# Kernel tuning notes

Measured on AMD Instinct MI355X. Metric: run time of the kernel, lower is better.

## Reference

```python
import jax, jax.numpy as jnp
import numpy as np

N = 50000          # number of input/output nodes (M == N since out_features=None)
E = 1_600_000      # total neighbor entries (avg degree 32)
C_IN = 64
HID = 128
C_OUT = 64


def setup_inputs() -> dict:
    key = jax.random.key(0)
    k1, k2, k3, k4, k5 = jax.random.split(key, 5)
    in_features = jax.random.normal(k1, (N, C_IN), dtype=jnp.float32)
    # MLP params: Linear(2C->HID), GELU, Linear(HID->C_OUT)
    W1 = jax.random.normal(k2, (2 * C_IN, HID), dtype=jnp.float32) * (1.0 / np.sqrt(2 * C_IN))
    b1 = jnp.zeros((HID,), dtype=jnp.float32)
    W2 = jax.random.normal(k3, (HID, C_OUT), dtype=jnp.float32) * (1.0 / np.sqrt(HID))
    b2 = jnp.zeros((C_OUT,), dtype=jnp.float32)
    neighbors_index = jax.random.randint(k4, (E,), 0, N, dtype=jnp.int64)
    # row_splits: sorted, starts at 0, ends at E (CSR-style ragged offsets)
    inner = jnp.sort(jax.random.randint(k5, (N - 1,), 0, E, dtype=jnp.int64))
    neighbors_row_splits = jnp.concatenate(
        [jnp.zeros((1,), jnp.int64), inner, jnp.full((1,), E, jnp.int64)])
    return {
        "in_features": in_features,
        "W1": W1, "b1": b1, "W2": W2, "b2": b2,
        "neighbors_index": neighbors_index,
        "neighbors_row_splits": neighbors_row_splits,
    }


def reference(in_features, W1, b1, W2, b2, neighbors_index, neighbors_row_splits):
    rs = neighbors_row_splits
    counts = rs[1:] - rs[:-1]                                  # [M] num_reps per row
    # segment id of each edge: row i owns edges [rs[i], rs[i+1])
    seg_ids = jnp.searchsorted(rs[1:], jnp.arange(E), side="right")  # [E]

    rep_features = in_features[neighbors_index]                # gather neighbors [E, C]
    self_features = in_features[seg_ids]                       # repeat_interleave  [E, C]
    agg = jnp.concatenate([rep_features, self_features], axis=1)  # [E, 2C]

    h = jax.nn.gelu(agg @ W1 + b1, approximate=False)          # torch GELU = exact erf
    msg = h @ W2 + b2                                          # [E, C_out]

    summed = jax.ops.segment_sum(msg, seg_ids, num_segments=N)  # [M, C_out]
    denom = jnp.maximum(counts, 1).astype(msg.dtype)[:, None]
    return summed / denom                                       # mean reduction
```

## Files before the change

kernel.cpp:

```cpp
#include <hip/hip_runtime.h>
#include <hip/hip_bf16.h>
#include <math.h>

#define C_IN  64
#define HID   128
#define C_OUT 64

typedef __attribute__((ext_vector_type(8))) short s16x8;
typedef __attribute__((ext_vector_type(4))) float f32x4;
typedef __attribute__((ext_vector_type(2))) float f32x2;

__device__ __forceinline__ f32x2 gelu2(f32x2 x) {
    f32x2 t  = x * x;
    f32x2 p  = t * 0.10294455f + 2.30211462f;
    f32x2 xp = x * p;
    f32x2 E;
    E.x = __builtin_amdgcn_exp2f(xp.x);
    E.y = __builtin_amdgcn_exp2f(xp.y);
    f32x2 Ep = E + 1.0f;
    f32x2 r;
    r.x = __builtin_amdgcn_rcpf(Ep.x);
    r.y = __builtin_amdgcn_rcpf(Ep.y);
    return x - x * r;
}

__device__ __forceinline__ float4 fma4(float s, float4 w, float4 acc) {
    acc.x = fmaf(s, w.x, acc.x); acc.y = fmaf(s, w.y, acc.y);
    acc.z = fmaf(s, w.z, acc.z); acc.w = fmaf(s, w.w, acc.w);
    return acc;
}

__device__ __forceinline__ unsigned pk_bf16(float lo, float hi) {
    union { __hip_bfloat162 v; unsigned u; } cv;
    cv.v = __float22bfloat162_rn(make_float2(lo, hi));
    return cv.u;
}
__device__ __forceinline__ f32x2 unpk2(unsigned p) {
    union { unsigned u; float f; } lo, hi;
    lo.u = p << 16; hi.u = p & 0xffff0000u;
    f32x2 v; v.x = lo.f; v.y = hi.f; return v;
}

#define K1_NODES 64

__global__ __launch_bounds__(512, 2) void precompute_ab(
    const float* __restrict__ X, const float* __restrict__ W1,
    const float* __restrict__ b1, const float* __restrict__ W2,
    const int* __restrict__ rs,
    unsigned* __restrict__ A16, float* __restrict__ B,
    unsigned short* __restrict__ W2T, int* __restrict__ bsplit,
    int N, int E, int G)
{
    __shared__ float W1s[2 * C_IN * HID];
    __shared__ float xs[K1_NODES * C_IN];
    int tid = threadIdx.x;

    for (int i = tid; i < (2 * C_IN * HID) / 4; i += 512)
        ((float4*)W1s)[i] = ((const float4*)W1)[i];

    int base = blockIdx.x * K1_NODES;
    int nLoc = min(K1_NODES, N - base);
    for (int i = tid; i < nLoc * (C_IN / 4); i += 512)
        ((float4*)xs)[i] = ((const float4*)(X + (size_t)base * C_IN))[i];

    if (blockIdx.x == 0) {
        for (int i = tid; i < C_OUT * HID; i += 512) {
            int c = i >> 7, k = i & (HID - 1);
            W2T[i] = (unsigned short)pk_bf16(W2[k * C_OUT + c], 0.f);
        }
    }

    {
        int gi = blockIdx.x * 512 + tid;
        if (gi <= G) {
            int t = (int)(((long long)E * gi) / G);
            int lo = 0, hi = N;
            while (lo < hi) { int mm = (lo + hi) >> 1; if (rs[mm] < t) lo = mm + 1; else hi = mm; }
            bsplit[gi] = lo;
        }
    }

    __syncthreads();

    int quad = (tid & 31) * 4;
    int slot = tid >> 5;
    int s0   = slot * 4;
    if (s0 >= nLoc) return;

    float4 a0 = {}, a1 = {}, a2 = {}, a3 = {};
    float4 b0 = {}, b1r = {}, b2r = {}, b3 = {};

    const float* xr0 = xs + (s0 + 0) * C_IN;
    const float* xr1 = xs + (s0 + 1) * C_IN;
    const float* xr2 = xs + (s0 + 2) * C_IN;
    const float* xr3 = xs + (s0 + 3) * C_IN;

#define K1STEP(c, CMP)                                                      \
    do {                                                                    \
        float4 wa = *(const float4*)&W1s[(c) * HID + quad];                 \
        float4 wb = *(const float4*)&W1s[((c) + C_IN) * HID + quad];        \
        a0 = fma4(xv0.CMP, wa, a0); b0  = fma4(xv0.CMP, wb, b0);            \
        a1 = fma4(xv1.CMP, wa, a1); b1r = fma4(xv1.CMP, wb, b1r);           \
        a2 = fma4(xv2.CMP, wa, a2); b2r = fma4(xv2.CMP, wb, b2r);           \
        a3 = fma4(xv3.CMP, wa, a3); b3  = fma4(xv3.CMP, wb, b3);            \
    } while (0)

#pragma unroll 1
    for (int c4 = 0; c4 < C_IN; c4 += 4) {
        float4 xv0 = *(const float4*)&xr0[c4];
        float4 xv1 = *(const float4*)&xr1[c4];
        float4 xv2 = *(const float4*)&xr2[c4];
        float4 xv3 = *(const float4*)&xr3[c4];
        K1STEP(c4 + 0, x);
        K1STEP(c4 + 1, y);
        K1STEP(c4 + 2, z);
        K1STEP(c4 + 3, w);
    }
#undef K1STEP

    float4 bb = *(const float4*)(b1 + quad);
    b0.x += bb.x;  b0.y += bb.y;  b0.z += bb.z;  b0.w += bb.w;
    b1r.x += bb.x; b1r.y += bb.y; b1r.z += bb.z; b1r.w += bb.w;
    b2r.x += bb.x; b2r.y += bb.y; b2r.z += bb.z; b2r.w += bb.w;
    b3.x += bb.x;  b3.y += bb.y;  b3.z += bb.z;  b3.w += bb.w;

    int adw = (base + s0) * (HID / 2) + (quad >> 1);
    size_t boff = (size_t)(base + s0) * HID + quad;
    if (s0 + 0 < nLoc) {
        uint2 u = { pk_bf16(a0.x, a0.y), pk_bf16(a0.z, a0.w) };
        *(uint2*)(A16 + adw) = u;              *(float4*)(B + boff) = b0;
    }
    if (s0 + 1 < nLoc) {
        uint2 u = { pk_bf16(a1.x, a1.y), pk_bf16(a1.z, a1.w) };
        *(uint2*)(A16 + adw + HID / 2) = u;    *(float4*)(B + boff + HID) = b1r;
    }
    if (s0 + 2 < nLoc) {
        uint2 u = { pk_bf16(a2.x, a2.y), pk_bf16(a2.z, a2.w) };
        *(uint2*)(A16 + adw + HID) = u;        *(float4*)(B + boff + 2 * HID) = b2r;
    }
    if (s0 + 3 < nLoc) {
        uint2 u = { pk_bf16(a3.x, a3.y), pk_bf16(a3.z, a3.w) };
        *(uint2*)(A16 + adw + 3 * (HID / 2)) = u; *(float4*)(B + boff + 3 * HID) = b3;
    }
}

#define EA_WAVES 2

#define EA_ISSUE(P0,P1,P2,P3, g) do { int _s8 = ((g) << 3) + half;            \
    int _i0 = __shfl(idx, _s8);                                               \
    int _i1 = __shfl(idx, _s8 + 2);                                           \
    int _i2 = __shfl(idx, _s8 + 4);                                           \
    int _i3 = __shfl(idx, _s8 + 6);                                           \
    P0 = *(const uint2*)(A8 + ((((unsigned)_i0) << 8) | lb));                 \
    P1 = *(const uint2*)(A8 + ((((unsigned)_i1) << 8) | lb));                 \
    P2 = *(const uint2*)(A8 + ((((unsigned)_i2) << 8) | lb));                 \
    P3 = *(const uint2*)(A8 + ((((unsigned)_i3) << 8) | lb));                 \
} while (0)

#define EA_PROC1(P) do {                                                      \
    acc01 += gelu2(unpk2(P.x) + bb01);                                        \
    acc23 += gelu2(unpk2(P.y) + bb23); } while (0)

#define EA_PROC1M(P, p) do {                                                  \
    float _mk = ((((p) << 1) + half) < m) ? 1.f : 0.f;                        \
    acc01 += gelu2(unpk2(P.x) + bb01) * _mk;                                  \
    acc23 += gelu2(unpk2(P.y) + bb23) * _mk; } while (0)

#define EA_PROCG(P0,P1,P2,P3, g) do {                                         \
    if ((((g) + 1) << 3) <= m) { EA_PROC1(P0); EA_PROC1(P1);                  \
                                 EA_PROC1(P2); EA_PROC1(P3); }                \
    else { int _p = (g) << 2;                                                 \
           EA_PROC1M(P0, _p);                                                 \
           if (((_p + 1) << 1) < m) EA_PROC1M(P1, _p + 1);                    \
           if (((_p + 2) << 1) < m) EA_PROC1M(P2, _p + 2);                    \
           if (((_p + 3) << 1) < m) EA_PROC1M(P3, _p + 3); } } while (0)

__global__ __launch_bounds__(128) void edge_agg(
    const unsigned* __restrict__ A16, const float* __restrict__ B,
    const int* __restrict__ nbr, const int* __restrict__ rs,
    const int* __restrict__ bsplit,
    unsigned* __restrict__ Hout, int N, int E, int G)
{
    int wave = threadIdx.x >> 6, lane = threadIdx.x & 63;
    int half = lane >> 5, l5 = lane & 31;
    const char* A8 = (const char*)A16;
    unsigned lb = (unsigned)(l5 << 3);
    int b = blockIdx.x;

    int r0 = bsplit[b];
    int r1 = (b == G - 1) ? N : bsplit[b + 1];

    int row = r0 + wave;
    if (row >= r1) return;

    int s = rs[row], e = rs[row + 1];
    float4 bb4 = *(const float4*)(B + (size_t)row * HID + l5 * 4);
    int idx = 0;
    if (e > s) { int mn = min(64, e - s); idx = nbr[s + min(lane, mn - 1)]; }

    for (;;) {
        int cnt = e - s;

        int nrow = row + EA_WAVES;
        bool hasn = nrow < r1;
        int sn = s, en = e;
        float4 bbn = bb4;
        if (hasn) {
            sn = rs[nrow]; en = rs[nrow + 1];
            bbn = *(const float4*)(B + (size_t)nrow * HID + l5 * 4);
        }

        f32x2 bb01, bb23;
        bb01.x = bb4.x; bb01.y = bb4.y; bb23.x = bb4.z; bb23.y = bb4.w;
        f32x2 acc01 = {0.f, 0.f}, acc23 = {0.f, 0.f};

        if (cnt > 0) {
            int cs = s;
            for (;;) {
                int m = min(64, e - cs);
                int ng = (m + 7) >> 3;

                uint2 A0, A1, A2, A3, B0, B1, B2, B3, C0, C1, C2, C3;
                EA_ISSUE(A0, A1, A2, A3, 0);
                if (ng > 1) EA_ISSUE(B0, B1, B2, B3, 1);

                int ncs = cs + 64;
                int idx_next = idx;
                if (ncs < e) {
                    int mn = min(64, e - ncs);
                    idx_next = nbr[ncs + min(lane, mn - 1)];
                } else if (hasn && en > sn) {
                    int mn = min(64, en - sn);
                    idx_next = nbr[sn + min(lane, mn - 1)];
                }

                int g = 0;
                for (;;) {
                    if (g + 2 < ng) EA_ISSUE(C0, C1, C2, C3, g + 2);
                    EA_PROCG(A0, A1, A2, A3, g);
                    if (++g >= ng) break;
                    if (g + 2 < ng) EA_ISSUE(A0, A1, A2, A3, g + 2);
                    EA_PROCG(B0, B1, B2, B3, g);
                    if (++g >= ng) break;
                    if (g + 2 < ng) EA_ISSUE(B0, B1, B2, B3, g + 2);
                    EA_PROCG(C0, C1, C2, C3, g);
                    if (++g >= ng) break;
                }

                idx = idx_next;
                if (ncs >= e) break;
                cs = ncs;
            }
        } else if (hasn && en > sn) {
            int mn = min(64, en - sn);
            idx = nbr[sn + min(lane, mn - 1)];
        }

        acc01.x += __shfl_xor(acc01.x, 32);
        acc01.y += __shfl_xor(acc01.y, 32);
        acc23.x += __shfl_xor(acc23.x, 32);
        acc23.y += __shfl_xor(acc23.y, 32);

        if (half == 0) {
            float sc = (cnt > 0) ? 1.f / (float)cnt : 0.f;
            uint2 o = { pk_bf16(acc01.x * sc, acc01.y * sc),
                        pk_bf16(acc23.x * sc, acc23.y * sc) };
            ((uint2*)(Hout + (size_t)row * (HID / 2)))[l5] = o;
        }

        if (!hasn) break;
        row = nrow; s = sn; e = en; bb4 = bbn;
    }
}

#undef EA_ISSUE
#undef EA_PROC1
#undef EA_PROC1M
#undef EA_PROCG

__global__ __launch_bounds__(256) void h_w2_mfma(
    const unsigned short* __restrict__ H, const unsigned short* __restrict__ W2T,
    const float* __restrict__ b2, const int* __restrict__ rs,
    float* __restrict__ out, int N)
{
    int wave = threadIdx.x >> 6, lane = threadIdx.x & 63;
    int base = (blockIdx.x * 4 + wave) * 16;
    if (base >= N) return;

    int r16 = lane & 15;
    int kg  = lane >> 4;

    const unsigned short* hrow = H + (size_t)(base + r16) * HID + kg * 8;
    const unsigned short* wc0  = W2T + (size_t)(0 * 16 + r16) * HID + kg * 8;
    const unsigned short* wc1  = W2T + (size_t)(1 * 16 + r16) * HID + kg * 8;
    const unsigned short* wc2  = W2T + (size_t)(2 * 16 + r16) * HID + kg * 8;
    const unsigned short* wc3  = W2T + (size_t)(3 * 16 + r16) * HID + kg * 8;

    f32x4 acc0 = {0.f, 0.f, 0.f, 0.f};
    f32x4 acc1 = acc0, acc2 = acc0, acc3 = acc0;

#pragma unroll
    for (int kk = 0; kk < 4; ++kk) {
        s16x8 a  = *(const s16x8*)(hrow + kk * 32);
        s16x8 f0 = *(const s16x8*)(wc0 + kk * 32);
        s16x8 f1 = *(const s16x8*)(wc1 + kk * 32);
        s16x8 f2 = *(const s16x8*)(wc2 + kk * 32);
        s16x8 f3 = *(const s16x8*)(wc3 + kk * 32);
        acc0 = __builtin_amdgcn_mfma_f32_16x16x32_bf16(a, f0, acc0, 0, 0, 0);
        acc1 = __builtin_amdgcn_mfma_f32_16x16x32_bf16(a, f1, acc1, 0, 0, 0);
        acc2 = __builtin_amdgcn_mfma_f32_16x16x32_bf16(a, f2, acc2, 0, 0, 0);
        acc3 = __builtin_amdgcn_mfma_f32_16x16x32_bf16(a, f3, acc3, 0, 0, 0);
    }

    float bia0 = b2[r16], bia1 = b2[16 + r16], bia2 = b2[32 + r16], bia3 = b2[48 + r16];

#pragma unroll
    for (int r = 0; r < 4; ++r) {
        int row = base + kg * 4 + r;
        if (row < N) {
            float mmk = (rs[row + 1] > rs[row]) ? 1.f : 0.f;
            float* o = out + (size_t)row * C_OUT;
            o[r16]      = mmk * (acc0[r] + bia0);
            o[16 + r16] = mmk * (acc1[r] + bia1);
            o[32 + r16] = mmk * (acc2[r] + bia2);
            o[48 + r16] = mmk * (acc3[r] + bia3);
        }
    }
}

extern "C" void kernel_launch(void* const* d_in, const int* in_sizes, int n_in,
                              void* d_out, int out_size, void* d_ws, size_t ws_size,
                              hipStream_t stream) {
    const float* X  = (const float*)d_in[0];
    const float* W1 = (const float*)d_in[1];
    const float* b1 = (const float*)d_in[2];
    const float* W2 = (const float*)d_in[3];
    const float* b2 = (const float*)d_in[4];
    const int*   nbr = (const int*)d_in[5];
    const int*   rs  = (const int*)d_in[6];
    float* outp = (float*)d_out;

    int N = in_sizes[6] - 1;
    int E = in_sizes[5];

    int G = 12288;

    unsigned*       A16  = (unsigned*)d_ws;
    float*          Bbuf = (float*)(A16 + (size_t)N * (HID / 2));
    unsigned*       Hout = (unsigned*)(Bbuf + (size_t)N * HID);
    unsigned short* W2T  = (unsigned short*)(Hout + (size_t)N * (HID / 2));
    int*            bsplit = (int*)(W2T + C_OUT * HID);

    int g1 = (N + K1_NODES - 1) / K1_NODES;
    hipLaunchKernelGGL(precompute_ab, dim3(g1), dim3(512), 0, stream,
                       X, W1, b1, W2, rs, A16, Bbuf, W2T, bsplit, N, E, G);

    hipLaunchKernelGGL(edge_agg, dim3(G), dim3(128), 0, stream,
                       A16, Bbuf, nbr, rs, bsplit, Hout, N, E, G);

    int stripes = (N + 15) / 16;
    int g3 = (stripes + 3) / 4;
    hipLaunchKernelGGL(h_w2_mfma, dim3(g3), dim3(256), 0, stream,
                       (const unsigned short*)Hout, W2T, b2, rs, outp, N);
}
```

Baseline: 129.3 us.

## Widen edge gather to 16-byte loads with four edges per wave step

```diff
diff --git a/kernel.cpp b/kernel.cpp
--- a/kernel.cpp
+++ b/kernel.cpp
@@ -146,45 +146,50 @@
 
 #define EA_WAVES 2
 
-#define EA_ISSUE(P0,P1,P2,P3, g) do { int _s8 = ((g) << 3) + half;            \
-    int _i0 = __shfl(idx, _s8);                                               \
-    int _i1 = __shfl(idx, _s8 + 2);                                           \
-    int _i2 = __shfl(idx, _s8 + 4);                                           \
-    int _i3 = __shfl(idx, _s8 + 6);                                           \
-    P0 = *(const uint2*)(A8 + ((((unsigned)_i0) << 8) | lb));                 \
-    P1 = *(const uint2*)(A8 + ((((unsigned)_i1) << 8) | lb));                 \
-    P2 = *(const uint2*)(A8 + ((((unsigned)_i2) << 8) | lb));                 \
-    P3 = *(const uint2*)(A8 + ((((unsigned)_i3) << 8) | lb));                 \
+#define EA_ISSUE(P0,P1,P2,P3, gc, IDX) do { int _b = ((gc) << 4) + q;         \
+    int _i0 = __shfl((IDX), _b);                                              \
+    int _i1 = __shfl((IDX), _b + 4);                                          \
+    int _i2 = __shfl((IDX), _b + 8);                                          \
+    int _i3 = __shfl((IDX), _b + 12);                                         \
+    P0 = *(const uint4*)(A8 + ((((unsigned)_i0) << 8) | lb));                 \
+    P1 = *(const uint4*)(A8 + ((((unsigned)_i1) << 8) | lb));                 \
+    P2 = *(const uint4*)(A8 + ((((unsigned)_i2) << 8) | lb));                 \
+    P3 = *(const uint4*)(A8 + ((((unsigned)_i3) << 8) | lb));                 \
 } while (0)
 
-#define EA_PROC1(P) do {                                                      \
+#define EA_P1(P) do {                                                         \
     acc01 += gelu2(unpk2(P.x) + bb01);                                        \
-    acc23 += gelu2(unpk2(P.y) + bb23); } while (0)
-
-#define EA_PROC1M(P, p) do {                                                  \
-    float _mk = ((((p) << 1) + half) < m) ? 1.f : 0.f;                        \
+    acc23 += gelu2(unpk2(P.y) + bb23);                                        \
+    acc45 += gelu2(unpk2(P.z) + bb45);                                        \
+    acc67 += gelu2(unpk2(P.w) + bb67); } while (0)
+
+#define EA_P1M(P, eb) do {                                                    \
+    float _mk = ((eb) + q < cnt) ? 1.f : 0.f;                                 \
     acc01 += gelu2(unpk2(P.x) + bb01) * _mk;                                  \
-    acc23 += gelu2(unpk2(P.y) + bb23) * _mk; } while (0)
+    acc23 += gelu2(unpk2(P.y) + bb23) * _mk;                                  \
+    acc45 += gelu2(unpk2(P.z) + bb45) * _mk;                                  \
+    acc67 += gelu2(unpk2(P.w) + bb67) * _mk; } while (0)
 
 #define EA_PROCG(P0,P1,P2,P3, g) do {                                         \
-    if ((((g) + 1) << 3) <= m) { EA_PROC1(P0); EA_PROC1(P1);                  \
-                                 EA_PROC1(P2); EA_PROC1(P3); }                \
-    else { int _p = (g) << 2;                                                 \
-           EA_PROC1M(P0, _p);                                                 \
-           if (((_p + 1) << 1) < m) EA_PROC1M(P1, _p + 1);                    \
-           if (((_p + 2) << 1) < m) EA_PROC1M(P2, _p + 2);                    \
-           if (((_p + 3) << 1) < m) EA_PROC1M(P3, _p + 3); } } while (0)
-
-__global__ __launch_bounds__(128) void edge_agg(
+    if ((((g) + 1) << 4) <= cnt) { EA_P1(P0); EA_P1(P1);                      \
+                                   EA_P1(P2); EA_P1(P3); }                    \
+    else { int _eb = (g) << 4;                                                \
+           EA_P1M(P0, _eb);                                                   \
+           if (_eb + 4  < cnt) EA_P1M(P1, _eb + 4);                           \
+           if (_eb + 8  < cnt) EA_P1M(P2, _eb + 8);                           \
+           if (_eb + 12 < cnt) EA_P1M(P3, _eb + 12); } } while (0)
+
+__global__ __launch_bounds__(128, 6) void edge_agg(
     const unsigned* __restrict__ A16, const float* __restrict__ B,
     const int* __restrict__ nbr, const int* __restrict__ rs,
     const int* __restrict__ bsplit,
     unsigned* __restrict__ Hout, int N, int E, int G)
 {
     int wave = threadIdx.x >> 6, lane = threadIdx.x & 63;
-    int half = lane >> 5, l5 = lane & 31;
+    int q  = lane >> 4;
+    int l4 = lane & 15;
     const char* A8 = (const char*)A16;
-    unsigned lb = (unsigned)(l5 << 3);
+    unsigned lb = (unsigned)(l4 << 4);
     int b = blockIdx.x;
 
     int r0 = bsplit[b];
@@ -194,88 +199,96 @@
     if (row >= r1) return;
 
     int s = rs[row], e = rs[row + 1];
-    float4 bb4 = *(const float4*)(B + (size_t)row * HID + l5 * 4);
-    int idx = 0;
-    if (e > s) { int mn = min(64, e - s); idx = nbr[s + min(lane, mn - 1)]; }
+    int cnt = e - s;
+    int idxCur = 0;
+    if (cnt > 0) { int mn = min(64, cnt); idxCur = nbr[s + min(lane, mn - 1)]; }
 
     for (;;) {
-        int cnt = e - s;
+        float4 bb4a = *(const float4*)(B + (size_t)row * HID + l4 * 8);
+        float4 bb4b = *(const float4*)(B + (size_t)row * HID + l4 * 8 + 4);
+        f32x2 bb01, bb23, bb45, bb67;
+        bb01.x = bb4a.x; bb01.y = bb4a.y; bb23.x = bb4a.z; bb23.y = bb4a.w;
+        bb45.x = bb4b.x; bb45.y = bb4b.y; bb67.x = bb4b.z; bb67.y = bb4b.w;
+        f32x2 acc01 = {0.f, 0.f}, acc23 = {0.f, 0.f};
+        f32x2 acc45 = {0.f, 0.f}, acc67 = {0.f, 0.f};
+
+        uint4 A0, A1, A2, A3, B0, B1, B2, B3;
+        int nG = 0, cLow = 0;
+        int idxNxt = idxCur;
+        if (cnt > 0) {
+            nG = (cnt + 15) >> 4;
+            EA_ISSUE(A0, A1, A2, A3, 0, idxCur);
+            if (nG > 1) EA_ISSUE(B0, B1, B2, B3, 1, idxCur);
+            if (cnt > 64) { int mn = min(64, cnt - 64);
+                            idxNxt = nbr[s + 64 + min(lane, mn - 1)]; }
+        }
 
         int nrow = row + EA_WAVES;
         bool hasn = nrow < r1;
-        int sn = s, en = e;
-        float4 bbn = bb4;
+        int sn = 0, cntn = 0, idxN0 = 0;
         if (hasn) {
-            sn = rs[nrow]; en = rs[nrow + 1];
-            bbn = *(const float4*)(B + (size_t)nrow * HID + l5 * 4);
-        }
-
-        f32x2 bb01, bb23;
-        bb01.x = bb4.x; bb01.y = bb4.y; bb23.x = bb4.z; bb23.y = bb4.w;
-        f32x2 acc01 = {0.f, 0.f}, acc23 = {0.f, 0.f};
+            sn = rs[nrow]; int en = rs[nrow + 1]; cntn = en - sn;
+            if (cntn > 0) { int mn = min(64, cntn);
+                            idxN0 = nbr[sn + min(lane, mn - 1)]; }
+        }
 
         if (cnt > 0) {
-            int cs = s;
+            int g = 0;
             for (;;) {
-                int m = min(64, e - cs);
-                int ng = (m + 7) >> 3;
-
-                uint2 A0, A1, A2, A3, B0, B1, B2, B3, C0, C1, C2, C3;
-                EA_ISSUE(A0, A1, A2, A3, 0);
-                if (ng > 1) EA_ISSUE(B0, B1, B2, B3, 1);
-
-                int ncs = cs + 64;
-                int idx_next = idx;
-                if (ncs < e) {
-                    int mn = min(64, e - ncs);
-                    idx_next = nbr[ncs + min(lane, mn - 1)];
-                } else if (hasn && en > sn) {
-                    int mn = min(64, en - sn);
-                    idx_next = nbr[sn + min(lane, mn - 1)];
+                EA_PROCG(A0, A1, A2, A3, g);
+                { int gp = g + 2;
+                  if (gp < nG) { int gc = gp & 3;
+                      int IDX = ((gp >> 2) != cLow) ? idxNxt : idxCur;
+                      EA_ISSUE(A0, A1, A2, A3, gc, IDX); } }
+                if (++g >= nG) break;
+                if ((g & 3) == 0) {
+                    idxCur = idxNxt; ++cLow;
+                    int nb = (cLow + 1) << 6;
+                    if (nb < cnt) { int mn = min(64, cnt - nb);
+                                    idxNxt = nbr[s + nb + min(lane, mn - 1)]; }
                 }
-
-                int g = 0;
-                for (;;) {
-                    if (g + 2 < ng) EA_ISSUE(C0, C1, C2, C3, g + 2);
-                    EA_PROCG(A0, A1, A2, A3, g);
-                    if (++g >= ng) break;
-                    if (g + 2 < ng) EA_ISSUE(A0, A1, A2, A3, g + 2);
-                    EA_PROCG(B0, B1, B2, B3, g);
-                    if (++g >= ng) break;
-                    if (g + 2 < ng) EA_ISSUE(B0, B1, B2, B3, g + 2);
-                    EA_PROCG(C0, C1, C2, C3, g);
-                    if (++g >= ng) break;
+                EA_PROCG(B0, B1, B2, B3, g);
+                { int gp = g + 2;
+                  if (gp < nG) { int gc = gp & 3;
+                      int IDX = ((gp >> 2) != cLow) ? idxNxt : idxCur;
+                      EA_ISSUE(B0, B1, B2, B3, gc, IDX); } }
+                if (++g >= nG) break;
+                if ((g & 3) == 0) {
+                    idxCur = idxNxt; ++cLow;
+                    int nb = (cLow + 1) << 6;
+                    if (nb < cnt) { int mn = min(64, cnt - nb);
+                                    idxNxt = nbr[s + nb + min(lane, mn - 1)]; }
                 }
-
-                idx = idx_next;
-                if (ncs >= e) break;
-                cs = ncs;
             }
-        } else if (hasn && en > sn) {
-            int mn = min(64, en - sn);
-            idx = nbr[sn + min(lane, mn - 1)];
-        }
-
-        acc01.x += __shfl_xor(acc01.x, 32);
-        acc01.y += __shfl_xor(acc01.y, 32);
-        acc23.x += __shfl_xor(acc23.x, 32);
-        acc23.y += __shfl_xor(acc23.y, 32);
-
-        if (half == 0) {
+        }
+
+        acc01.x += __shfl_xor(acc01.x, 16); acc01.x += __shfl_xor(acc01.x, 32);
+        acc01.y += __shfl_xor(acc01.y, 16); acc01.y += __shfl_xor(acc01.y, 32);
+        acc23.x += __shfl_xor(acc23.x, 16); acc23.x += __shfl_xor(acc23.x, 32);
+        acc23.y += __shfl_xor(acc23.y, 16); acc23.y += __shfl_xor(acc23.y, 32);
+        acc45.x += __shfl_xor(acc45.x, 16); acc45.x += __shfl_xor(acc45.x, 32);
+        acc45.y += __shfl_xor(acc45.y, 16); acc45.y += __shfl_xor(acc45.y, 32);
+        acc67.x += __shfl_xor(acc67.x, 16); acc67.x += __shfl_xor(acc67.x, 32);
+        acc67.y += __shfl_xor(acc67.y, 16); acc67.y += __shfl_xor(acc67.y, 32);
+
+        if (q == 0) {
             float sc = (cnt > 0) ? 1.f / (float)cnt : 0.f;
-            uint2 o = { pk_bf16(acc01.x * sc, acc01.y * sc),
-                        pk_bf16(acc23.x * sc, acc23.y * sc) };
-            ((uint2*)(Hout + (size_t)row * (HID / 2)))[l5] = o;
+            uint4 o;
+            o.x = pk_bf16(acc01.x * sc, acc01.y * sc);
+            o.y = pk_bf16(acc23.x * sc, acc23.y * sc);
+            o.z = pk_bf16(acc45.x * sc, acc45.y * sc);
+            o.w = pk_bf16(acc67.x * sc, acc67.y * sc);
+            *((uint4*)(Hout + (size_t)row * (HID / 2)) + l4) = o;
         }
 
         if (!hasn) break;
-        row = nrow; s = sn; e = en; bb4 = bbn;
+        row = nrow; s = sn; cnt = cntn; idxCur = idxN0;
     }
 }
 
 #undef EA_ISSUE
-#undef EA_PROC1
-#undef EA_PROC1M
+#undef EA_P1
+#undef EA_P1M
 #undef EA_PROCG
 
 __global__ __launch_bounds__(256) void h_w2_mfma(
@@ -316,10 +329,10 @@
 
 #pragma unroll
     for (int r = 0; r < 4; ++r) {
-        int row = base + kg * 4 + r;
-        if (row < N) {
-            float mmk = (rs[row + 1] > rs[row]) ? 1.f : 0.f;
-            float* o = out + (size_t)row * C_OUT;
+        int rowi = base + kg * 4 + r;
+        if (rowi < N) {
+            float mmk = (rs[rowi + 1] > rs[rowi]) ? 1.f : 0.f;
+            float* o = out + (size_t)rowi * C_OUT;
             o[r16]      = mmk * (acc0[r] + bia0);
             o[16 + r16] = mmk * (acc1[r] + bia1);
             o[32 + r16] = mmk * (acc2[r] + bia2);
@@ -343,7 +356,7 @@
     int N = in_sizes[6] - 1;
     int E = in_sizes[5];
 
-    int G = 12288;
+    int G = 3072;
 
     unsigned*       A16  = (unsigned*)d_ws;
     float*          Bbuf = (float*)(A16 + (size_t)N * (HID / 2));
```

New measurement: 155.8 us. +20.6%, slower.
